# Performance work log

Measured on AMD Instinct MI355X. Metric: run time of the kernel, lower is better.

## Reference

```python
import jax, jax.numpy as jnp
from jax import lax
import numpy as np

N_GROUP = 1024   # number of FPS centroids
N_SAMPLE = 32    # neighbors per ball query
RADIUS = 0.2
BN_EPS = 1e-5    # torch BatchNorm2d default, training-mode batch stats
MLP = [64, 64, 128]
IN_CH = 6        # 3 relative xyz + 3 point features


def setup_inputs() -> dict:
    key = jax.random.key(0)
    ks = jax.random.split(key, 8)
    B, N = 16, 4096
    out = {
        "xyz": jax.random.uniform(ks[0], (B, N, 3), dtype=jnp.float32),
        "point_feature": jax.random.normal(ks[1], (B, N, 3), dtype=jnp.float32),
    }
    last = IN_CH
    for li, oc in enumerate(MLP):
        out[f"w{li}"] = jax.random.normal(ks[2 + li], (oc, last), dtype=jnp.float32) / np.float32(np.sqrt(last))
        out[f"b{li}"] = jnp.zeros((oc,), jnp.float32)
        out[f"g{li}"] = jnp.ones((oc,), jnp.float32)
        out[f"be{li}"] = jnp.zeros((oc,), jnp.float32)
        last = oc
    return out


def _fps(xyz, n_group):
    # Farthest point sampling. xyz: [B, N, 3] -> idx [B, n_group]
    B, N, _ = xyz.shape

    def step(carry, _):
        dist, farthest = carry                      # [B,N], [B]
        centroid = jnp.take_along_axis(xyz, farthest[:, None, None], axis=1)  # [B,1,3]
        d = jnp.sum((xyz - centroid) ** 2, -1)      # [B,N]
        dist = jnp.minimum(dist, d)
        nxt = jnp.argmax(dist, -1).astype(jnp.int32)
        return (dist, nxt), farthest

    init = (jnp.full((B, N), 1e10, xyz.dtype), jnp.zeros((B,), jnp.int32))
    _, idxs = lax.scan(step, init, None, length=n_group)
    return idxs.T                                    # [B, n_group]


def _ball_query(xyz, new_xyz, radius, n_sample):
    # xyz: [B,N,3], new_xyz: [B,S,3] -> idx [B,S,n_sample]
    B, N, _ = xyz.shape
    sqr = jnp.sum((new_xyz[:, :, None, :] - xyz[:, None, :, :]) ** 2, -1)  # [B,S,N]
    idx = jnp.where(sqr > radius * radius, N, jnp.arange(N, dtype=jnp.int32))
    idx = jnp.sort(idx, axis=-1)[:, :, :n_sample]    # closest-index fill like torch impl
    first = idx[:, :, :1]
    return jnp.where(idx == N, first, idx)


def reference(xyz, point_feature, w0, b0, g0, be0, w1, b1, g1, be1, w2, b2, g2, be2):
    B = xyz.shape[0]
    fps_idx = _fps(xyz, N_GROUP)                     # [B,S]
    bi = jnp.arange(B)[:, None]
    new_xyz = xyz[bi, fps_idx]                       # [B,S,3]

    idx = _ball_query(xyz, new_xyz, RADIUS, N_SAMPLE)  # [B,S,K]
    bii = jnp.arange(B)[:, None, None]
    grouped_xyz = xyz[bii, idx] - new_xyz[:, :, None, :]   # [B,S,K,3] centered
    grouped_feat = point_feature[bii, idx]                 # [B,S,K,3]
    x = jnp.concatenate([grouped_xyz, grouped_feat], -1)   # [B,S,K,6]

    # 1x1 Conv2d == per-point linear; BN over all dims but channel (training stats)
    for w, b, g, be in ((w0, b0, g0, be0), (w1, b1, g1, be1), (w2, b2, g2, be2)):
        x = jnp.einsum('bskc,oc->bsko', x, w) + b
        mu = x.mean((0, 1, 2))
        var = x.var((0, 1, 2))
        x = g * (x - mu) * lax.rsqrt(var + BN_EPS) + be
        x = jax.nn.relu(x)

    new_feature = x.max(axis=2)                      # max over n_sample -> [B,S,128]
    return new_xyz, new_feature
```

## Files before the change

### kernel.cpp

```cpp
#include <hip/hip_runtime.h>
#include <hip/hip_bf16.h>

constexpr int BATCH = 16;
constexpr int NPT   = 4096;
constexpr int NGRP  = 1024;
constexpr int NSMP  = 32;
constexpr int NPTS  = BATCH * NGRP * NSMP;
constexpr int PBLK  = 4096;
constexpr int NG    = BATCH * NGRP;

typedef __attribute__((ext_vector_type(2))) float f32x2;

__device__ __forceinline__ float sqd(float dx, float dy, float dz) {
  return __fadd_rn(__fadd_rn(__fmul_rn(dx, dx), __fmul_rn(dy, dy)), __fmul_rn(dz, dz));
}

template <int CTRL, int RM>
__device__ __forceinline__ unsigned long long dpp_lvl(unsigned long long P) {
  const int lo = (int)(unsigned int)P;
  const int hi = (int)(unsigned int)(P >> 32);
  const int tlo = __builtin_amdgcn_update_dpp(lo, lo, CTRL, RM, 0xF, false);
  const int thi = __builtin_amdgcn_update_dpp(hi, hi, CTRL, RM, 0xF, false);
  const unsigned long long T =
      ((unsigned long long)(unsigned int)thi << 32) | (unsigned int)tlo;
  return (T > P) ? T : P;
}

__global__ __launch_bounds__(256) void fps_kernel(const float* __restrict__ xyz,
                                                  float* __restrict__ out) {
  __shared__ float sx[NPT], sy[NPT], sz[NPT];
  __shared__ float cq[NGRP * 3];
  __shared__ unsigned int ex[2][5][4];
  const int b = blockIdx.x;
  const int t = threadIdx.x;
  const float* src = xyz + (size_t)b * NPT * 3;
  for (int i = t; i < NPT; i += 256) {
    sx[i] = src[i * 3 + 0];
    sy[i] = src[i * 3 + 1];
    sz[i] = src[i * 3 + 2];
  }
  __syncthreads();
  f32x2 px[8], py[8], pz[8], dist[8];
  #pragma unroll
  for (int m = 0; m < 8; ++m) {
    const int p0 = (2 * m) * 256 + t;
    const int p1 = (2 * m + 1) * 256 + t;
    px[m] = f32x2{sx[p0], sx[p1]};
    py[m] = f32x2{sy[p0], sy[p1]};
    pz[m] = f32x2{sz[p0], sz[p1]};
    dist[m] = f32x2{1e10f, 1e10f};
  }
  const int w = t >> 6;
  float cx = sx[0], cy = sy[0], cz = sz[0];
  for (int step = 0; step < NGRP; ++step) {
    if (t == 0) {
      cq[step * 3 + 0] = cx;
      cq[step * 3 + 1] = cy;
      cq[step * 3 + 2] = cz;
    }
    float bestd = -1.0f; int bi = 0x7fffffff;
    const f32x2 c2x = {cx, cx}, c2y = {cy, cy}, c2z = {cz, cz};
    #pragma unroll
    for (int m = 0; m < 8; ++m) {
      f32x2 d2;
      {
        #pragma clang fp contract(off)
        const f32x2 dx = px[m] - c2x;
        const f32x2 dy = py[m] - c2y;
        const f32x2 dz = pz[m] - c2z;
        d2 = (dx * dx + dy * dy) + dz * dz;
      }
      const float d0 = fminf(dist[m].x, d2.x);
      const float d1 = fminf(dist[m].y, d2.y);
      dist[m].x = d0;
      dist[m].y = d1;
      if (d0 > bestd) { bestd = d0; bi = (2 * m) * 256 + t; }
      if (d1 > bestd) { bestd = d1; bi = (2 * m + 1) * 256 + t; }
    }
    const int myidx = bi;
    const unsigned long long myP =
        ((unsigned long long)__float_as_uint(bestd) << 32) |
        (unsigned long long)(unsigned int)~myidx;
    const float mx = sx[myidx], my_ = sy[myidx], mz = sz[myidx];
    unsigned long long P = myP;
    P = dpp_lvl<0xB1, 0xF>(P);
    P = dpp_lvl<0x4E, 0xF>(P);
    P = dpp_lvl<0x141, 0xF>(P);
    P = dpp_lvl<0x140, 0xF>(P);
    P = dpp_lvl<0x142, 0xA>(P);
    P = dpp_lvl<0x143, 0xC>(P);
    const unsigned int flo = (unsigned int)__builtin_amdgcn_readlane((int)(unsigned int)P, 63);
    const unsigned int fhi =
        (unsigned int)__builtin_amdgcn_readlane((int)(unsigned int)(P >> 32), 63);
    const unsigned long long PF = ((unsigned long long)fhi << 32) | flo;
    const int pb = step & 1;
    if (myP == PF) {
      ex[pb][0][w] = fhi;
      ex[pb][1][w] = flo;
      ex[pb][2][w] = __float_as_uint(mx);
      ex[pb][3][w] = __float_as_uint(my_);
      ex[pb][4][w] = __float_as_uint(mz);
    }
    __syncthreads();
    const unsigned int* e = &ex[pb][0][0];
    unsigned long long best = ((unsigned long long)e[0] << 32) | e[4];
    cx = __uint_as_float(e[8]);
    cy = __uint_as_float(e[12]);
    cz = __uint_as_float(e[16]);
    #pragma unroll
    for (int k = 1; k < 4; ++k) {
      const unsigned long long pk_ = ((unsigned long long)e[k] << 32) | e[4 + k];
      if (pk_ > best) {
        best = pk_;
        cx = __uint_as_float(e[8 + k]);
        cy = __uint_as_float(e[12 + k]);
        cz = __uint_as_float(e[16 + k]);
      }
    }
  }
  __syncthreads();
  float* outx = out + (size_t)b * NGRP * 3;
  for (int i = t; i < NGRP * 3; i += 256) outx[i] = cq[i];
}

__global__ __launch_bounds__(256) void ballq_kernel(const float* __restrict__ xyz,
                                                    const float* __restrict__ pf,
                                                    const float* __restrict__ out,
                                                    int* __restrict__ idxg,
                                                    float* __restrict__ part) {
  __shared__ float sx[NPT], sy[NPT], sz[NPT];
  __shared__ int   sel[64 * NSMP];
  __shared__ float cent[64][3];
  const int b = blockIdx.x >> 4;
  const int sub = blockIdx.x & 15;
  const float* src = xyz + (size_t)b * NPT * 3;
  for (int i = threadIdx.x; i < NPT; i += 256) {
    sx[i] = src[i * 3 + 0];
    sy[i] = src[i * 3 + 1];
    sz[i] = src[i * 3 + 2];
  }
  __syncthreads();
  const int lane = threadIdx.x & 63;
  const int w = threadIdx.x >> 6;
  const float R2 = __fmul_rn(0.2f, 0.2f);
  for (int gi = 0; gi < 16; ++gi) {
    const int g = w * 16 + gi;
    const int s = sub * 64 + g;
    const float* c = out + ((size_t)b * NGRP + s) * 3;
    const float nx = c[0], ny = c[1], nz = c[2];
    if (lane == 0) { cent[g][0] = nx; cent[g][1] = ny; cent[g][2] = nz; }
    int* og = idxg + ((size_t)b * NGRP + s) * NSMP;
    int* sg = sel + g * NSMP;
    int cnt = 0, firstP = -1;
    for (int base = 0; base < NPT; base += 64) {
      const int p = base + lane;
      const float dsq = sqd(nx - sx[p], ny - sy[p], nz - sz[p]);
      const bool inr = (dsq <= R2);
      unsigned long long m = __ballot(inr);
      if (firstP < 0 && m) firstP = base + (int)__builtin_ctzll(m);
      const int rank = (int)__popcll(m & ((1ull << lane) - 1ull));
      if (inr) {
        const int pos = cnt + rank;
        if (pos < NSMP) { og[pos] = p; sg[pos] = p; }
      }
      cnt += (int)__popcll(m);
      if (cnt >= NSMP) break;
    }
    if (cnt < NSMP) {
      for (int pos = cnt + lane; pos < NSMP; pos += 64) { og[pos] = firstP; sg[pos] = firstP; }
    }
  }
  __syncthreads();
  float acc[27];
  #pragma unroll
  for (int k = 0; k < 27; ++k) acc[k] = 0.0f;
  const float* pfb = pf + (size_t)b * NPT * 3;
  const int g2 = threadIdx.x >> 2;
  const float c0 = cent[g2][0], c1 = cent[g2][1], c2 = cent[g2][2];
  #pragma unroll
  for (int ii = 0; ii < 8; ++ii) {
    const int si = threadIdx.x * 8 + ii;
    const int i = sel[si];
    float in[6];
    in[0] = sx[i] - c0;
    in[1] = sy[i] - c1;
    in[2] = sz[i] - c2;
    in[3] = pfb[i * 3 + 0];
    in[4] = pfb[i * 3 + 1];
    in[5] = pfb[i * 3 + 2];
    #pragma unroll
    for (int k = 0; k < 6; ++k) acc[k] += in[k];
    int k = 6;
    #pragma unroll
    for (int a = 0; a < 6; ++a)
      #pragma unroll
      for (int bb = a; bb < 6; ++bb) { acc[k] = fmaf(in[a], in[bb], acc[k]); ++k; }
  }
  #pragma unroll
  for (int off = 1; off < 64; off <<= 1) {
    #pragma unroll
    for (int k = 0; k < 27; ++k) acc[k] += __shfl_xor(acc[k], off);
  }
  if (lane == 0) {
    const int slot = blockIdx.x * 4 + w;
    #pragma unroll
    for (int k = 0; k < 27; ++k) part[k * 1024 + slot] = acc[k];
  }
}

__global__ void transpose_w3(const float* __restrict__ w3, float* __restrict__ w3t) {
  const int i = blockIdx.x * 256 + threadIdx.x;
  if (i < 128 * 64) {
    const int o = i >> 6, c = i & 63;
    w3t[c * 128 + o] = w3[i];
  }
}

__device__ __forceinline__ void gather6(const float* __restrict__ xyz, const float* __restrict__ pf,
                                        const float* __restrict__ nxyz, const int* __restrict__ idxg,
                                        int tid, float in[6]) {
  const int g = tid >> 5;
  const int b = g >> 10;
  const int i = idxg[tid];
  const float* P = xyz + ((size_t)b * NPT + i) * 3;
  const float* C = nxyz + (size_t)g * 3;
  in[0] = P[0] - C[0];
  in[1] = P[1] - C[1];
  in[2] = P[2] - C[2];
  const float* F = pf + ((size_t)b * NPT + i) * 3;
  in[3] = F[0]; in[4] = F[1]; in[5] = F[2];
}

__device__ __forceinline__ void layer1h(const float in[6], const float* __restrict__ w1,
                                        const float* __restrict__ b1, const float* __restrict__ ss1,
                                        float h1[64]) {
  #pragma unroll
  for (int o = 0; o < 64; ++o) {
    float a = b1[o];
    #pragma unroll
    for (int cc = 0; cc < 6; ++cc) a = fmaf(in[cc], w1[o * 6 + cc], a);
    h1[o] = fmaxf(0.0f, fmaf(a, ss1[o], ss1[64 + o]));
  }
}

__device__ __forceinline__ void zb_stats64(const float* zb, float* __restrict__ part,
                                           int chbase, int nch, int t, int blk) {
  const int c = t >> 1, h = t & 1;
  const float* row = zb + c * 129 + h * 64;
  float s = 0.0f, q = 0.0f;
  for (int i = 0; i < 64; ++i) {
    const float v = row[i];
    s += v;
    q = fmaf(v, v, q);
  }
  s += __shfl_xor(s, 1);
  q += __shfl_xor(q, 1);
  if (h == 0) {
    part[(size_t)(chbase + c) * PBLK + blk]       = s;
    part[(size_t)(nch + chbase + c) * PBLK + blk] = q;
  }
}

__device__ __forceinline__ void zb_stats_mm(const float* zb, float* __restrict__ part,
                                            float* __restrict__ pmax, float* __restrict__ pmin,
                                            int chbase, int nch, int t, int blk) {
  const int c = t >> 1, h = t & 1;
  const float* row = zb + c * 129 + h * 64;
  float s = 0.0f, q = 0.0f;
  float mx0 = -3.4e38f, mn0 = 3.4e38f, mx1 = -3.4e38f, mn1 = 3.4e38f;
  for (int i = 0; i < 32; ++i) {
    const float v = row[i];
    s += v; q = fmaf(v, v, q);
    mx0 = fmaxf(mx0, v); mn0 = fminf(mn0, v);
  }
  for (int i = 32; i < 64; ++i) {
    const float v = row[i];
    s += v; q = fmaf(v, v, q);
    mx1 = fmaxf(mx1, v); mn1 = fminf(mn1, v);
  }
  s += __shfl_xor(s, 1);
  q += __shfl_xor(q, 1);
  if (h == 0) {
    part[(size_t)(chbase + c) * PBLK + blk]       = s;
    part[(size_t)(nch + chbase + c) * PBLK + blk] = q;
  }
  const size_t g0 = (size_t)blk * 4 + 2 * h;
  pmax[g0 * 128 + chbase + c]       = mx0;
  pmax[(g0 + 1) * 128 + chbase + c] = mx1;
  pmin[g0 * 128 + chbase + c]       = mn0;
  pmin[(g0 + 1) * 128 + chbase + c] = mn1;
}

__global__ __launch_bounds__(256) void momred_kernel(const float* __restrict__ part,
                                                     double* __restrict__ dsum, int n) {
  const int c = blockIdx.x;
  const int t = threadIdx.x;
  double s = 0.0;
  for (int i = t; i < n; i += 256) s += (double)part[c * n + i];
  #pragma unroll
  for (int off = 1; off < 64; off <<= 1) s += __shfl_xor(s, off);
  __shared__ double ls[4];
  const int lane = t & 63, w = t >> 6;
  if (lane == 0) ls[w] = s;
  __syncthreads();
  if (t == 0) dsum[c] = ls[0] + ls[1] + ls[2] + ls[3];
}

__global__ __launch_bounds__(64) void finalize1_kernel(const double* __restrict__ dsum,
                                                       const float* __restrict__ w1,
                                                       const float* __restrict__ b1,
                                                       const float* __restrict__ g,
                                                       const float* __restrict__ be,
                                                       float* __restrict__ ss) {
  __shared__ double sm[27];
  const int t = threadIdx.x;
  if (t < 27) sm[t] = dsum[t];
  __syncthreads();
  const double N = (double)NPTS;
  double wv[6];
  #pragma unroll
  for (int i = 0; i < 6; ++i) wv[i] = (double)w1[t * 6 + i];
  double mean_wx = 0.0;
  #pragma unroll
  for (int i = 0; i < 6; ++i) mean_wx += wv[i] * sm[i];
  mean_wx /= N;
  const double bb = (double)b1[t];
  const double mu = mean_wx + bb;
  double qq = 0.0;
  int k = 6;
  #pragma unroll
  for (int i = 0; i < 6; ++i)
    #pragma unroll
    for (int j = i; j < 6; ++j) {
      qq += (i == j ? 1.0 : 2.0) * wv[i] * wv[j] * (sm[k] / N);
      ++k;
    }
  const double Ez2 = qq + 2.0 * bb * mean_wx + bb * bb;
  const double var = Ez2 - mu * mu;
  const double inv = 1.0 / sqrt(var + 1e-5);
  ss[t]      = (float)((double)g[t] * inv);
  ss[64 + t] = (float)((double)be[t] - (double)g[t] * mu * inv);
}

__global__ __launch_bounds__(256) void reduce_kernel(const float* __restrict__ part, int nblk, int nch,
                                                     const float* __restrict__ g, const float* __restrict__ be,
                                                     float* __restrict__ ss) {
  const int c = blockIdx.x;
  const int t = threadIdx.x;
  double s = 0.0, q = 0.0;
  for (int i = t; i < nblk; i += 256) {
    s += (double)part[(size_t)c * nblk + i];
    q += (double)part[(size_t)(nch + c) * nblk + i];
  }
  #pragma unroll
  for (int off = 1; off < 64; off <<= 1) {
    s += __shfl_xor(s, off);
    q += __shfl_xor(q, off);
  }
  __shared__ double ls[4], lq[4];
  const int lane = t & 63, w = t >> 6;
  if (lane == 0) { ls[w] = s; lq[w] = q; }
  __syncthreads();
  if (t == 0) {
    const double S = ls[0] + ls[1] + ls[2] + ls[3];
    const double Q = lq[0] + lq[1] + lq[2] + lq[3];
    const double n = (double)NPTS;
    const double mu = S / n;
    const double var = Q / n - mu * mu;
    const double inv = 1.0 / sqrt(var + 1e-5);
    ss[c]       = (float)((double)g[c] * inv);
    ss[nch + c] = (float)((double)be[c] - (double)g[c] * mu * inv);
  }
}

__global__ __launch_bounds__(128) void pass2_kernel(const float* __restrict__ xyz, const float* __restrict__ pf,
                                                    const float* __restrict__ nxyz, const int* __restrict__ idxg,
                                                    const float* __restrict__ w1, const float* __restrict__ b1,
                                                    const float* __restrict__ ss1,
                                                    const float* __restrict__ w2, const float* __restrict__ b2,
                                                    float* __restrict__ part,
                                                    __hip_bfloat16* __restrict__ z2c) {
  __shared__ float zb[64 * 129];
  const int t = threadIdx.x;
  const int tid = blockIdx.x * 128 + t;
  float in[6];
  gather6(xyz, pf, nxyz, idxg, tid, in);
  float h1[64];
  layer1h(in, w1, b1, ss1, h1);
  for (int o = 0; o < 64; ++o) {
    float a = b2[o];
    #pragma unroll
    for (int cc = 0; cc < 64; ++cc) a = fmaf(h1[cc], w2[o * 64 + cc], a);
    zb[o * 129 + t] = a;
    if (z2c) z2c[(size_t)o * NPTS + tid] = __float2bfloat16(a);
  }
  __syncthreads();
  zb_stats64(zb, part, 0, 64, t, blockIdx.x);
}

__device__ __forceinline__ void compute_z3(const float* __restrict__ xyz, const float* __restrict__ pf,
                                           const float* __restrict__ nxyz, const int* __restrict__ idxg,
                                           const float* __restrict__ w1, const float* __restrict__ b1,
                                           const float* __restrict__ ss1,
                                           const float* __restrict__ w2, const float* __restrict__ b2,
                                           const float* __restrict__ ss2,
                                           const float* __restrict__ w3t, const float* __restrict__ b3,
                                           const __hip_bfloat16* __restrict__ z2c,
                                           float* shm, int t, int tid, float acc[128]) {
  float* hrow = shm + t * 65;
  if (z2c) {
    #pragma unroll
    for (int o = 0; o < 64; ++o) {
      const float z = __bfloat162float(z2c[(size_t)o * NPTS + tid]);
      hrow[o] = fmaxf(0.0f, fmaf(z, ss2[o], ss2[64 + o]));
    }
  } else {
    float in[6];
    gather6(xyz, pf, nxyz, idxg, tid, in);
    float h1[64];
    layer1h(in, w1, b1, ss1, h1);
    for (int o = 0; o < 64; ++o) {
      float a = b2[o];
      #pragma unroll
      for (int cc = 0; cc < 64; ++cc) a = fmaf(h1[cc], w2[o * 64 + cc], a);
      hrow[o] = fmaxf(0.0f, fmaf(a, ss2[o], ss2[64 + o]));
    }
  }
  #pragma unroll
  for (int o = 0; o < 128; ++o) acc[o] = b3[o];
  for (int cc = 0; cc < 64; ++cc) {
    const float hc = hrow[cc];
    const float* wrow = w3t + cc * 128;
    #pragma unroll
    for (int o = 0; o < 128; ++o) acc[o] = fmaf(hc, wrow[o], acc[o]);
  }
}

__global__ __launch_bounds__(128) void pass3_kernel(const float* __restrict__ xyz, const float* __restrict__ pf,
                                                    const float* __restrict__ nxyz, const int* __restrict__ idxg,
                                                    const float* __restrict__ w1, const float* __restrict__ b1,
                                                    const float* __restrict__ ss1,
                                                    const float* __restrict__ w2, const float* __restrict__ b2,
                                                    const float* __restrict__ ss2,
                                                    const float* __restrict__ w3t, const float* __restrict__ b3,
                                                    const __hip_bfloat16* __restrict__ z2c,
                                                    float* __restrict__ part,
                                                    float* __restrict__ pmax, float* __restrict__ pmin) {
  __shared__ float shm[8320];
  const int t = threadIdx.x;
  const int tid = blockIdx.x * 128 + t;
  float acc[128];
  compute_z3(xyz, pf, nxyz, idxg, w1, b1, ss1, w2, b2, ss2, w3t, b3, z2c, shm, t, tid, acc);
  __syncthreads();
  #pragma unroll
  for (int o = 0; o < 64; ++o) shm[o * 129 + t] = acc[o];
  __syncthreads();
  if (pmax) zb_stats_mm(shm, part, pmax, pmin, 0, 128, t, blockIdx.x);
  else      zb_stats64(shm, part, 0, 128, t, blockIdx.x);
  __syncthreads();
  #pragma unroll
  for (int o = 0; o < 64; ++o) shm[o * 129 + t] = acc[64 + o];
  __syncthreads();
  if (pmax) zb_stats_mm(shm, part, pmax, pmin, 64, 128, t, blockIdx.x);
  else      zb_stats64(shm, part, 64, 128, t, blockIdx.x);
}

__global__ __launch_bounds__(256) void pass4f_kernel(const float* __restrict__ pmax,
                                                     const float* __restrict__ pmin,
                                                     const float* __restrict__ ss3,
                                                     float* __restrict__ outF) {
  const int i = blockIdx.x * 256 + threadIdx.x;
  const int c = i & 127;
  const float a = ss3[c], bb = ss3[128 + c];
  const float z = (a >= 0.0f) ? pmax[i] : pmin[i];
  outF[i] = fmaxf(0.0f, fmaf(z, a, bb));
}

__global__ __launch_bounds__(128) void pass4_kernel(const float* __restrict__ xyz, const float* __restrict__ pf,
                                                    const float* __restrict__ nxyz, const int* __restrict__ idxg,
                                                    const float* __restrict__ w1, const float* __restrict__ b1,
                                                    const float* __restrict__ ss1,
                                                    const float* __restrict__ w2, const float* __restrict__ b2,
                                                    const float* __restrict__ ss2,
                                                    const float* __restrict__ w3t, const float* __restrict__ b3,
                                                    const __hip_bfloat16* __restrict__ z2c,
                                                    const float* __restrict__ ss3,
                                                    float* __restrict__ outF) {
  __shared__ float shm[8320];
  const int t = threadIdx.x;
  const int tid = blockIdx.x * 128 + t;
  float acc[128];
  compute_z3(xyz, pf, nxyz, idxg, w1, b1, ss1, w2, b2, ss2, w3t, b3, z2c, shm, t, tid, acc);
  #pragma unroll
  for (int o = 0; o < 128; ++o)
    acc[o] = fmaxf(0.0f, fmaf(acc[o], ss3[o], ss3[128 + o]));
  __syncthreads();
  const int c4 = t & 63, gp = t >> 6;
  #pragma unroll
  for (int o = 0; o < 64; ++o) shm[o * 129 + t] = acc[o];
  __syncthreads();
  #pragma unroll
  for (int gs = 0; gs < 2; ++gs) {
    const int g = gp * 2 + gs;
    const float* row = shm + c4 * 129 + g * 32;
    float m = row[0];
    for (int i = 1; i < 32; ++i) m = fmaxf(m, row[i]);
    outF[((size_t)blockIdx.x * 4 + g) * 128 + c4] = m;
  }
  __syncthreads();
  #pragma unroll
  for (int o = 0; o < 64; ++o) shm[o * 129 + t] = acc[64 + o];
  __syncthreads();
  #pragma unroll
  for (int gs = 0; gs < 2; ++gs) {
    const int g = gp * 2 + gs;
    const float* row = shm + c4 * 129 + g * 32;
    float m = row[0];
    for (int i = 1; i < 32; ++i) m = fmaxf(m, row[i]);
    outF[((size_t)blockIdx.x * 4 + g) * 128 + 64 + c4] = m;
  }
}

extern "C" void kernel_launch(void* const* d_in, const int* in_sizes, int n_in,
                              void* d_out, int out_size, void* d_ws, size_t ws_size,
                              hipStream_t stream) {
  (void)in_sizes; (void)n_in; (void)out_size;
  const float* xyz = (const float*)d_in[0];
  const float* pf  = (const float*)d_in[1];
  const float* w1  = (const float*)d_in[2];
  const float* b1  = (const float*)d_in[3];
  const float* g1  = (const float*)d_in[4];
  const float* be1 = (const float*)d_in[5];
  const float* w2  = (const float*)d_in[6];
  const float* b2  = (const float*)d_in[7];
  const float* g2  = (const float*)d_in[8];
  const float* be2 = (const float*)d_in[9];
  const float* w3  = (const float*)d_in[10];
  const float* b3  = (const float*)d_in[11];
  const float* g3  = (const float*)d_in[12];
  const float* be3 = (const float*)d_in[13];
  float* out = (float*)d_out;

  int*    idxg = (int*)d_ws;
  float*  p1   = (float*)((char*)d_ws + (size_t)NPTS * 4);
  float*  ss1  = p1 + (size_t)PBLK * 128;
  float*  p2   = ss1 + 128;
  float*  ss2  = p2 + (size_t)PBLK * 128;
  float*  p3   = ss2 + 128;
  float*  ss3  = p3 + (size_t)PBLK * 256;
  float*  w3t  = ss3 + 256;
  double* dsum = (double*)(w3t + 8192);
  float*  pmax = (float*)(dsum + 32);
  float*  pmin = pmax + (size_t)NG * 128;
  __hip_bfloat16* z2c = (__hip_bfloat16*)(pmin + (size_t)NG * 128);
  const size_t needed4 = (size_t)((char*)z2c - (char*)d_ws);
  const size_t needed3 = needed4 + (size_t)NPTS * 64 * sizeof(__hip_bfloat16);
  const bool fast4 = (ws_size >= needed4);
  const bool fast3 = (ws_size >= needed3);
  __hip_bfloat16* z2cp = fast3 ? z2c : nullptr;

  transpose_w3<<<32, 256, 0, stream>>>(w3, w3t);
  fps_kernel<<<BATCH, 256, 0, stream>>>(xyz, out);
  ballq_kernel<<<BATCH * 16, 256, 0, stream>>>(xyz, pf, out, idxg, p1);
  momred_kernel<<<27, 256, 0, stream>>>(p1, dsum, 1024);
  finalize1_kernel<<<1, 64, 0, stream>>>(dsum, w1, b1, g1, be1, ss1);
  pass2_kernel<<<PBLK, 128, 0, stream>>>(xyz, pf, out, idxg, w1, b1, ss1, w2, b2, p2, z2cp);
  reduce_kernel<<<64, 256, 0, stream>>>(p2, PBLK, 64, g2, be2, ss2);
  pass3_kernel<<<PBLK, 128, 0, stream>>>(xyz, pf, out, idxg, w1, b1, ss1, w2, b2, ss2, w3t, b3, z2cp,
                                         p3, fast4 ? pmax : nullptr, fast4 ? pmin : nullptr);
  reduce_kernel<<<128, 256, 0, stream>>>(p3, PBLK, 128, g3, be3, ss3);
  float* outF = out + (size_t)BATCH * NGRP * 3;
  if (fast4) {
    pass4f_kernel<<<(NG * 128) / 256, 256, 0, stream>>>(pmax, pmin, ss3, outF);
  } else {
    pass4_kernel<<<PBLK, 128, 0, stream>>>(xyz, pf, out, idxg, w1, b1, ss1, w2, b2, ss2, w3t, b3,
                                           z2cp, ss3, outF);
  }
}
```

Before: 1.181 ms.

## Run FPS with a single wavefront per batch to remove block barriers

```diff
diff --git a/kernel.cpp b/kernel.cpp
--- a/kernel.cpp
+++ b/kernel.cpp
@@ -26,31 +26,29 @@
   return (T > P) ? T : P;
 }
 
-__global__ __launch_bounds__(256) void fps_kernel(const float* __restrict__ xyz,
-                                                  float* __restrict__ out) {
+__global__ __launch_bounds__(64) void fps_kernel(const float* __restrict__ xyz,
+                                                 float* __restrict__ out) {
   __shared__ float sx[NPT], sy[NPT], sz[NPT];
   __shared__ float cq[NGRP * 3];
-  __shared__ unsigned int ex[2][5][4];
   const int b = blockIdx.x;
   const int t = threadIdx.x;
   const float* src = xyz + (size_t)b * NPT * 3;
-  for (int i = t; i < NPT; i += 256) {
+  for (int i = t; i < NPT; i += 64) {
     sx[i] = src[i * 3 + 0];
     sy[i] = src[i * 3 + 1];
     sz[i] = src[i * 3 + 2];
   }
   __syncthreads();
-  f32x2 px[8], py[8], pz[8], dist[8];
-  #pragma unroll
-  for (int m = 0; m < 8; ++m) {
-    const int p0 = (2 * m) * 256 + t;
-    const int p1 = (2 * m + 1) * 256 + t;
+  f32x2 px[32], py[32], pz[32], dist[32];
+  #pragma unroll
+  for (int m = 0; m < 32; ++m) {
+    const int p0 = (2 * m) * 64 + t;
+    const int p1 = (2 * m + 1) * 64 + t;
     px[m] = f32x2{sx[p0], sx[p1]};
     py[m] = f32x2{sy[p0], sy[p1]};
     pz[m] = f32x2{sz[p0], sz[p1]};
     dist[m] = f32x2{1e10f, 1e10f};
   }
-  const int w = t >> 6;
   float cx = sx[0], cy = sy[0], cz = sz[0];
   for (int step = 0; step < NGRP; ++step) {
     if (t == 0) {
@@ -61,7 +59,7 @@
     float bestd = -1.0f; int bi = 0x7fffffff;
     const f32x2 c2x = {cx, cx}, c2y = {cy, cy}, c2z = {cz, cz};
     #pragma unroll
-    for (int m = 0; m < 8; ++m) {
+    for (int m = 0; m < 32; ++m) {
       f32x2 d2;
       {
         #pragma clang fp contract(off)
@@ -74,15 +72,12 @@
       const float d1 = fminf(dist[m].y, d2.y);
       dist[m].x = d0;
       dist[m].y = d1;
-      if (d0 > bestd) { bestd = d0; bi = (2 * m) * 256 + t; }
-      if (d1 > bestd) { bestd = d1; bi = (2 * m + 1) * 256 + t; }
-    }
-    const int myidx = bi;
-    const unsigned long long myP =
+      if (d0 > bestd) { bestd = d0; bi = (2 * m) * 64 + t; }
+      if (d1 > bestd) { bestd = d1; bi = (2 * m + 1) * 64 + t; }
+    }
+    unsigned long long P =
         ((unsigned long long)__float_as_uint(bestd) << 32) |
-        (unsigned long long)(unsigned int)~myidx;
-    const float mx = sx[myidx], my_ = sy[myidx], mz = sz[myidx];
-    unsigned long long P = myP;
+        (unsigned long long)(unsigned int)~bi;
     P = dpp_lvl<0xB1, 0xF>(P);
     P = dpp_lvl<0x4E, 0xF>(P);
     P = dpp_lvl<0x141, 0xF>(P);
@@ -90,37 +85,14 @@
     P = dpp_lvl<0x142, 0xA>(P);
     P = dpp_lvl<0x143, 0xC>(P);
     const unsigned int flo = (unsigned int)__builtin_amdgcn_readlane((int)(unsigned int)P, 63);
-    const unsigned int fhi =
-        (unsigned int)__builtin_amdgcn_readlane((int)(unsigned int)(P >> 32), 63);
-    const unsigned long long PF = ((unsigned long long)fhi << 32) | flo;
-    const int pb = step & 1;
-    if (myP == PF) {
-      ex[pb][0][w] = fhi;
-      ex[pb][1][w] = flo;
-      ex[pb][2][w] = __float_as_uint(mx);
-      ex[pb][3][w] = __float_as_uint(my_);
-      ex[pb][4][w] = __float_as_uint(mz);
-    }
-    __syncthreads();
-    const unsigned int* e = &ex[pb][0][0];
-    unsigned long long best = ((unsigned long long)e[0] << 32) | e[4];
-    cx = __uint_as_float(e[8]);
-    cy = __uint_as_float(e[12]);
-    cz = __uint_as_float(e[16]);
-    #pragma unroll
-    for (int k = 1; k < 4; ++k) {
-      const unsigned long long pk_ = ((unsigned long long)e[k] << 32) | e[4 + k];
-      if (pk_ > best) {
-        best = pk_;
-        cx = __uint_as_float(e[8 + k]);
-        cy = __uint_as_float(e[12 + k]);
-        cz = __uint_as_float(e[16 + k]);
-      }
-    }
+    const unsigned int myidx = ~flo;
+    cx = sx[myidx];
+    cy = sy[myidx];
+    cz = sz[myidx];
   }
   __syncthreads();
   float* outx = out + (size_t)b * NGRP * 3;
-  for (int i = t; i < NGRP * 3; i += 256) outx[i] = cq[i];
+  for (int i = t; i < NGRP * 3; i += 64) outx[i] = cq[i];
 }
 
 __global__ __launch_bounds__(256) void ballq_kernel(const float* __restrict__ xyz,
@@ -560,7 +532,7 @@
   __hip_bfloat16* z2cp = fast3 ? z2c : nullptr;
 
   transpose_w3<<<32, 256, 0, stream>>>(w3, w3t);
-  fps_kernel<<<BATCH, 256, 0, stream>>>(xyz, out);
+  fps_kernel<<<BATCH, 64, 0, stream>>>(xyz, out);
   ballq_kernel<<<BATCH * 16, 256, 0, stream>>>(xyz, pf, out, idxg, p1);
   momred_kernel<<<27, 256, 0, stream>>>(p1, dsum, 1024);
   finalize1_kernel<<<1, 64, 0, stream>>>(dsum, w1, b1, g1, be1, ss1);
```

Measured after the change: 2.048 ms. 73.4% more time.
